# Kernel optimization log

Hardware: AMD Instinct MI355X
Metric: run time of the kernel (lower is better)

## Reference

```python
import jax, jax.numpy as jnp
import numpy as np

NUM_GROUPS = 32
NUM_HEADS = 8
EPS = 1e-5


def group_norm(x, gamma, beta):
    B, C, H, W = x.shape
    g = NUM_GROUPS
    xg = x.reshape(B, g, C // g, H, W)
    mean = xg.mean(axis=(2, 3, 4), keepdims=True)
    var = xg.var(axis=(2, 3, 4), keepdims=True)
    xn = ((xg - mean) * jax.lax.rsqrt(var + EPS)).reshape(B, C, H, W)
    return xn * gamma[None, :, None, None] + beta[None, :, None, None]


def setup_inputs() -> dict:
    key = jax.random.key(0)
    ks = jax.random.split(key, 7)
    B, C, H, W = 16, 512, 32, 32
    x = jax.random.normal(ks[0], (B, C, H, W), dtype=jnp.float32)
    norm_w = jnp.ones((C,), jnp.float32)
    norm_b = jnp.zeros((C,), jnp.float32)
    s1 = 1.0 / np.sqrt(C)
    qkv_w = jax.random.uniform(ks[1], (3 * C, C), jnp.float32, -s1, s1)
    qkv_b = jax.random.uniform(ks[2], (3 * C,), jnp.float32, -s1, s1)
    proj_w = jax.random.uniform(ks[3], (C, C), jnp.float32, -s1, s1)
    proj_b = jax.random.uniform(ks[4], (C,), jnp.float32, -s1, s1)
    return {"x": x, "norm_w": norm_w, "norm_b": norm_b,
            "qkv_w": qkv_w, "qkv_b": qkv_b,
            "proj_w": proj_w, "proj_b": proj_b}


def reference(x, norm_w, norm_b, qkv_w, qkv_b, proj_w, proj_b):
    B, C, H, W = x.shape
    nh = NUM_HEADS
    hd = C // nh
    S = H * W
    h = group_norm(x, norm_w, norm_b)
    # 1x1 conv == channel matmul: [B,3C,H,W]
    qkv = jnp.einsum('oc,bchw->bohw', qkv_w, h) + qkv_b[None, :, None, None]
    q, k, v = jnp.split(qkv, 3, axis=1)
    # q,v -> [B, nh, S, hd]; k -> [B, nh, hd, S]
    q = q.reshape(B, nh, hd, S).transpose(0, 1, 3, 2)
    k = k.reshape(B, nh, hd, S)
    v = v.reshape(B, nh, hd, S).transpose(0, 1, 3, 2)
    scale = 1.0 / np.sqrt(hd)
    attn = jnp.einsum('bhsd,bhdt->bhst', q, k) * scale
    attn = jax.nn.softmax(attn, axis=-1)
    out = jnp.einsum('bhst,bhtd->bhsd', attn, v)  # [B,nh,S,hd]
    out = out.transpose(0, 1, 3, 2).reshape(B, C, H, W)
    out = jnp.einsum('oc,bchw->bohw', proj_w, out) + proj_b[None, :, None, None]
    return out + x
```

## Files before the change

kernel.cpp:

```cpp
#include <hip/hip_runtime.h>
#include <hip/hip_bf16.h>
#include <stdint.h>

#define B_N 16
#define C_N 512
#define S_N 1024
#define G_N 32
#define NH  8
#define HD  64

typedef __attribute__((ext_vector_type(8))) short bf16x8;
typedef __attribute__((ext_vector_type(4))) float f32x4;
typedef __attribute__((ext_vector_type(16))) float f32x16;
typedef unsigned short u16;
typedef unsigned int   u32;
typedef __attribute__((ext_vector_type(4))) u16 u16x4;
typedef __attribute__((ext_vector_type(4))) u32 u32x4;

#define SC2F 0.18033688011112042f

__device__ __forceinline__ u16 f2bf(float f) {
  u32 u = __builtin_bit_cast(u32, f);
  u32 r = (u + 0x7fffu + ((u >> 16) & 1u)) >> 16;
  return (u16)r;
}

__device__ __forceinline__ u32 cvtpk(float a, float b) {
  u32 r;
  asm("v_cvt_pk_bf16_f32 %0, %1, %2" : "=v"(r) : "v"(a), "v"(b));
  return r;
}

__device__ __forceinline__ void gll16(const void* g, void* l) {
  __builtin_amdgcn_global_load_lds((const __attribute__((address_space(1))) u32*)g,
                                   (__attribute__((address_space(3))) u32*)l, 16, 0, 0);
}

__global__ __launch_bounds__(256) void gn_stats_cvt(const float* __restrict__ x,
                                                    float* __restrict__ stats,
                                                    const float* __restrict__ qkvw,
                                                    const float* __restrict__ projw,
                                                    u16* __restrict__ qw,
                                                    u16* __restrict__ pw) {
  const int blk = blockIdx.x;
  if (blk < 512) {
    const int bg = blk;
    const float4* xv = (const float4*)(x + (size_t)bg * (16 * S_N));
    float s = 0.f, ss = 0.f;
    for (int i = threadIdx.x; i < 4096; i += 256) {
      float4 v = xv[i];
      s  += v.x + v.y + v.z + v.w;
      ss += v.x*v.x + v.y*v.y + v.z*v.z + v.w*v.w;
    }
    #pragma unroll
    for (int m = 1; m < 64; m <<= 1) { s += __shfl_xor(s, m); ss += __shfl_xor(ss, m); }
    __shared__ float red[2][4];
    const int wid = threadIdx.x >> 6;
    if ((threadIdx.x & 63) == 0) { red[0][wid] = s; red[1][wid] = ss; }
    __syncthreads();
    if (threadIdx.x == 0) {
      float S1 = red[0][0]+red[0][1]+red[0][2]+red[0][3];
      float S2 = red[1][0]+red[1][1]+red[1][2]+red[1][3];
      float mean = S1 * (1.f/16384.f);
      float var  = S2 * (1.f/16384.f) - mean*mean;
      stats[bg*2]   = mean;
      stats[bg*2+1] = rsqrtf(var + 1e-5f);
    }
  } else {
    int i = (blk - 512)*256 + threadIdx.x;
    const float4* src; u16x4* dst; int j;
    if (i < 196608) { src = (const float4*)qkvw;  dst = (u16x4*)qw; j = i; }
    else            { src = (const float4*)projw; dst = (u16x4*)pw; j = i - 196608; }
    float4 v = src[j];
    u16x4 r = { f2bf(v.x), f2bf(v.y), f2bf(v.z), f2bf(v.w) };
    dst[j] = r;
  }
}

__global__ __launch_bounds__(256) void gn_apply_t(const float* __restrict__ x,
                                                  const float* __restrict__ stats,
                                                  const float* __restrict__ nw,
                                                  const float* __restrict__ nb,
                                                  u16* __restrict__ h_t) {
  const int c0 = blockIdx.x * 32, s0 = blockIdx.y * 64, b = blockIdx.z;
  __shared__ u16 tile[32][68];
  const int t = threadIdx.x;
  #pragma unroll
  for (int i = 0; i < 2; i++) {
    int idx4 = (i*256 + t) * 4;
    int cr = idx4 >> 6, sr = idx4 & 63;
    int c = c0 + cr;
    float4 v = *(const float4*)&x[((size_t)b*C_N + c)*S_N + s0 + sr];
    int bg = b*G_N + (c >> 4);
    float mean = stats[bg*2], rstd = stats[bg*2+1];
    float w = nw[c]*rstd;
    float bb = nb[c] - mean*w;
    tile[cr][sr]   = f2bf(v.x*w + bb);
    tile[cr][sr+1] = f2bf(v.y*w + bb);
    tile[cr][sr+2] = f2bf(v.z*w + bb);
    tile[cr][sr+3] = f2bf(v.w*w + bb);
  }
  __syncthreads();
  #pragma unroll
  for (int i = 0; i < 2; i++) {
    int idx = i*256 + t;
    int sr = idx >> 3;
    int cr4 = (idx & 7) * 4;
    u16x4 v = { tile[cr4][sr], tile[cr4+1][sr], tile[cr4+2][sr], tile[cr4+3][sr] };
    *(u16x4*)&h_t[((size_t)b*S_N + s0 + sr)*C_N + c0 + cr4] = v;
  }
}

__global__ __launch_bounds__(256) void gemm_qkv(const u16* __restrict__ h_t,
                                                const u16* __restrict__ wq,
                                                const float* __restrict__ bq,
                                                u16* __restrict__ Qp,
                                                u16* __restrict__ Kp,
                                                u16* __restrict__ Vp) {
  __shared__ u16 Ash[2][128*32];
  __shared__ u16 Bsh[2][128*32];
  const int n0 = blockIdx.x*128, m0 = blockIdx.y*128, b = blockIdx.z;
  const int tid = threadIdx.x, wid = tid >> 6, lane = tid & 63;
  const int wm = wid >> 1, wn = wid & 1;
  const u16* Ag = h_t + (size_t)b*S_N*C_N;
  const f32x4 vzero = {0.f,0.f,0.f,0.f};
  f32x4 acc[4][4];
  #pragma unroll
  for (int i=0;i<4;i++)
    #pragma unroll
    for (int j=0;j<4;j++) acc[i][j] = vzero;

  const int arow = lane >> 2, aslot = (lane & 3) * 8;

  auto stage = [&](u16* Adst, u16* Bdst, int k0s) {
    #pragma unroll
    for (int i = 0; i < 2; i++) {
      int r = wid*32 + i*16 + arow;
      gll16(Ag + (size_t)(m0+r)*C_N + k0s + aslot, &Adst[(wid*32+i*16)*32]);
      gll16(wq + (size_t)(n0+r)*C_N + k0s + aslot, &Bdst[(wid*32+i*16)*32]);
    }
  };
  auto compute = [&](const u16* AshC, const u16* BshC) {
    bf16x8 aF[4], bF[4];
    #pragma unroll
    for (int mi=0;mi<4;mi++)
      aF[mi] = *(const bf16x8*)&AshC[(wm*64+mi*16+(lane&15))*32 + (lane>>4)*8];
    #pragma unroll
    for (int ni=0;ni<4;ni++)
      bF[ni] = *(const bf16x8*)&BshC[(wn*64+ni*16+(lane&15))*32 + (lane>>4)*8];
    #pragma unroll
    for (int mi=0;mi<4;mi++)
      #pragma unroll
      for (int ni=0;ni<4;ni++)
        acc[mi][ni] = __builtin_amdgcn_mfma_f32_16x16x32_bf16(aF[mi], bF[ni], acc[mi][ni], 0, 0, 0);
  };

  stage(Ash[0], Bsh[0], 0);
  #pragma unroll 1
  for (int k0 = 0; k0 < C_N; k0 += 64) {
    asm volatile("s_waitcnt vmcnt(0)" ::: "memory");
    __syncthreads();
    stage(Ash[1], Bsh[1], k0 + 32);
    compute(Ash[0], Bsh[0]);
    asm volatile("s_waitcnt vmcnt(0)" ::: "memory");
    __syncthreads();
    if (k0 + 64 < C_N) stage(Ash[0], Bsh[0], k0 + 64);
    compute(Ash[1], Bsh[1]);
  }

  #pragma unroll
  for (int mi=0;mi<4;mi++) {
    #pragma unroll
    for (int ni=0;ni<4;ni++) {
      int o = n0 + wn*64 + ni*16 + (lane & 15);
      float bias = bq[o];
      int sec = o >> 9;
      int oo  = o & 511;
      int hh  = oo >> 6, d = oo & 63;
      size_t bh = (size_t)(b*NH + hh);
      float qsc = (sec == 0) ? SC2F : 1.0f;
      #pragma unroll
      for (int r=0;r<4;r++) {
        int s = m0 + wm*64 + mi*16 + (lane>>4)*4 + r;
        u16 bv = f2bf((acc[mi][ni][r] + bias) * qsc);
        if (sec == 0)      Qp[(bh*S_N + s)*HD + d] = bv;
        else if (sec == 1) Kp[(bh*S_N + s)*HD + d] = bv;
        else               Vp[(bh*HD + d)*S_N + s] = bv;
      }
    }
  }
}

__device__ __forceinline__ void attn_tile_body(const u16* __restrict__ Kb,
                                               const u16* __restrict__ Vb,
                                               const u16* __restrict__ KlC, const u16* __restrict__ VlC,
                                               u16* __restrict__ KlN, u16* __restrict__ VlN,
                                               const bf16x8 (&qf)[4], const bf16x8 onesf,
                                               f32x16 (&oacc)[2], f32x16& oacc_l,
                                               const int (&off)[2][4],
                                               int it, int hi,
                                               int ra, int rb, int ca, int cb, int wid) {
  const int t0 = it * 64;
  asm volatile("s_waitcnt vmcnt(0)" ::: "memory");
  __syncthreads();

  if (it < 15) {
    const int tn = t0 + 64;
    gll16(Kb + (size_t)(tn + ra)*HD + ca, &KlN[(wid*16    )*64]);
    gll16(Kb + (size_t)(tn + rb)*HD + cb, &KlN[(wid*16 + 8)*64]);
    gll16(Vb + (size_t)ra*S_N + tn + ca,  &VlN[(wid*16    )*64]);
    gll16(Vb + (size_t)rb*S_N + tn + cb,  &VlN[(wid*16 + 8)*64]);
  }

  bf16x8 kF[2][4];
  #pragma unroll
  for (int tt=0;tt<2;tt++)
    #pragma unroll
    for (int kt=0;kt<4;kt++)
      kF[tt][kt] = *(const bf16x8*)&KlC[off[tt][kt]];

  f32x16 st[2];
  #pragma unroll
  for (int tt=0;tt<2;tt++)
    #pragma unroll
    for (int i=0;i<16;i++) st[tt][i] = 0.f;
  __builtin_amdgcn_s_setprio(1);
  #pragma unroll
  for (int tt=0;tt<2;tt++)
    #pragma unroll
    for (int kt=0;kt<4;kt++)
      st[tt] = __builtin_amdgcn_mfma_f32_32x32x16_bf16(kF[tt][kt], qf[kt], st[tt], 0, 0, 0);
  __builtin_amdgcn_s_setprio(0);

  #pragma unroll
  for (int tt=0;tt<2;tt++)
    #pragma unroll
    for (int i=0;i<16;i++)
      st[tt][i] = exp2f(st[tt][i]);

  u32x4 paw[4];
  #pragma unroll
  for (int ks=0;ks<4;ks++) {
    u32 w0 = cvtpk(st[ks>>1][(ks&1)*8+0], st[ks>>1][(ks&1)*8+1]);
    u32 w1 = cvtpk(st[ks>>1][(ks&1)*8+2], st[ks>>1][(ks&1)*8+3]);
    u32 w2 = cvtpk(st[ks>>1][(ks&1)*8+4], st[ks>>1][(ks&1)*8+5]);
    u32 w3 = cvtpk(st[ks>>1][(ks&1)*8+6], st[ks>>1][(ks&1)*8+7]);
    asm("v_permlane32_swap_b32 %0, %1" : "+v"(w0), "+v"(w2));
    asm("v_permlane32_swap_b32 %0, %1" : "+v"(w1), "+v"(w3));
    u32x4 w = { w0, w1, w2, w3 };
    paw[ks] = w;
  }

  __builtin_amdgcn_s_setprio(1);
  #pragma unroll
  for (int ks=0;ks<4;ks++) {
    bf16x8 pb = __builtin_bit_cast(bf16x8, paw[ks]);
    oacc_l = __builtin_amdgcn_mfma_f32_32x32x16_bf16(onesf, pb, oacc_l, 0, 0, 0);
    #pragma unroll
    for (int dt=0;dt<2;dt++) {
      bf16x8 vF = *(const bf16x8*)&VlC[off[dt][ks]];
      oacc[dt] = __builtin_amdgcn_mfma_f32_32x32x16_bf16(vF, pb, oacc[dt], 0, 0, 0);
    }
  }
  __builtin_amdgcn_s_setprio(0);
}

__global__ __launch_bounds__(256) void attn_fwd(const u16* __restrict__ Qp,
                                                const u16* __restrict__ Kp,
                                                const u16* __restrict__ Vp,
                                                u16* __restrict__ at) {
  __shared__ u16 Kl[2][64*64];
  __shared__ u16 Vl[2][64*64];
  const int hh = blockIdx.x, q0 = blockIdx.y*128, b = blockIdx.z;
  const int tid = threadIdx.x, wid = tid >> 6, lane = tid & 63;
  const int l31 = lane & 31, hi = lane >> 5;
  const size_t bh = (size_t)(b*NH + hh);
  const u16* Qb = Qp + bh*(S_N*HD);
  const u16* Kb = Kp + bh*(S_N*HD);
  const u16* Vb = Vp + bh*(HD*S_N);
  const int s = q0 + wid*32 + l31;

  bf16x8 qf[4];
  #pragma unroll
  for (int kt=0;kt<4;kt++)
    qf[kt] = *(const bf16x8*)&Qb[(size_t)s*HD + kt*16 + hi*8];

  const u32x4 onesw = {0x3F803F80u, 0x3F803F80u, 0x3F803F80u, 0x3F803F80u};
  const bf16x8 onesf = __builtin_bit_cast(bf16x8, onesw);

  f32x16 oacc[2], oacc_l;
  #pragma unroll
  for (int dt=0;dt<2;dt++)
    #pragma unroll
    for (int i=0;i<16;i++) oacc[dt][i] = 0.f;
  #pragma unroll
  for (int i=0;i<16;i++) oacc_l[i] = 0.f;

  int off[2][4];
  #pragma unroll
  for (int g=0; g<2; g++)
    #pragma unroll
    for (int kt=0; kt<4; kt++) {
      int row = g*32 + l31;
      int phys = (kt*2 + hi) ^ (row & 7);
      off[g][kt] = row*64 + phys*8;
    }

  const int ra = wid*16 + (lane >> 3);
  const int rb = ra + 8;
  const int ca = (((lane & 7) ^ (ra & 7)) * 8);
  const int cb = (((lane & 7) ^ (rb & 7)) * 8);

  gll16(Kb + (size_t)ra*HD + ca,  &Kl[0][(wid*16    )*64]);
  gll16(Kb + (size_t)rb*HD + cb,  &Kl[0][(wid*16 + 8)*64]);
  gll16(Vb + (size_t)ra*S_N + ca, &Vl[0][(wid*16    )*64]);
  gll16(Vb + (size_t)rb*S_N + cb, &Vl[0][(wid*16 + 8)*64]);

  #pragma unroll 1
  for (int it = 0; it < 16; it += 2) {
    attn_tile_body(Kb, Vb, Kl[0], Vl[0], Kl[1], Vl[1], qf, onesf, oacc, oacc_l, off,
                   it,     hi, ra, rb, ca, cb, wid);
    attn_tile_body(Kb, Vb, Kl[1], Vl[1], Kl[0], Vl[0], qf, onesf, oacc, oacc_l, off,
                   it + 1, hi, ra, rb, ca, cb, wid);
  }

  float inv = 1.0f / oacc_l[0];
  #pragma unroll
  for (int dt=0;dt<2;dt++)
    #pragma unroll
    for (int qd=0;qd<4;qd++) {
      int dbase = 4*hi + 8*qd + 32*dt;
      u16x4 o;
      #pragma unroll
      for (int j=0;j<4;j++) o[j] = f2bf(oacc[dt][qd*4+j] * inv);
      *(u16x4*)&at[((size_t)b*S_N + s)*C_N + hh*HD + dbase] = o;
    }
}

__global__ __launch_bounds__(256) void gemm_proj(const u16* __restrict__ pwb,
                                                 const u16* __restrict__ at,
                                                 const float* __restrict__ bp,
                                                 const float* __restrict__ x,
                                                 float* __restrict__ out) {
  __shared__ u16 Ash[2][128*32];
  __shared__ u16 Bsh[2][128*32];
  const int n0 = blockIdx.x*128, m0 = blockIdx.y*128, b = blockIdx.z;
  const int tid = threadIdx.x, wid = tid >> 6, lane = tid & 63;
  const int wm = wid >> 1, wn = wid & 1;
  const u16* Bg = at + (size_t)b*S_N*C_N;
  const f32x4 vzero = {0.f,0.f,0.f,0.f};
  f32x4 acc[4][4];
  #pragma unroll
  for (int i=0;i<4;i++)
    #pragma unroll
    for (int j=0;j<4;j++) acc[i][j] = vzero;

  const int arow = lane >> 2, aslot = (lane & 3) * 8;

  auto stage = [&](u16* Adst, u16* Bdst, int k0s) {
    #pragma unroll
    for (int i = 0; i < 2; i++) {
      int r = wid*32 + i*16 + arow;
      gll16(pwb + (size_t)(m0+r)*C_N + k0s + aslot, &Adst[(wid*32+i*16)*32]);
      gll16(Bg  + (size_t)(n0+r)*C_N + k0s + aslot, &Bdst[(wid*32+i*16)*32]);
    }
  };
  auto compute = [&](const u16* AshC, const u16* BshC) {
    bf16x8 aF[4], bF[4];
    #pragma unroll
    for (int mi=0;mi<4;mi++)
      aF[mi] = *(const bf16x8*)&AshC[(wm*64+mi*16+(lane&15))*32 + (lane>>4)*8];
    #pragma unroll
    for (int ni=0;ni<4;ni++)
      bF[ni] = *(const bf16x8*)&BshC[(wn*64+ni*16+(lane&15))*32 + (lane>>4)*8];
    #pragma unroll
    for (int mi=0;mi<4;mi++)
      #pragma unroll
      for (int ni=0;ni<4;ni++)
        acc[mi][ni] = __builtin_amdgcn_mfma_f32_16x16x32_bf16(aF[mi], bF[ni], acc[mi][ni], 0, 0, 0);
  };

  stage(Ash[0], Bsh[0], 0);
  #pragma unroll 1
  for (int k0 = 0; k0 < C_N; k0 += 64) {
    asm volatile("s_waitcnt vmcnt(0)" ::: "memory");
    __syncthreads();
    stage(Ash[1], Bsh[1], k0 + 32);
    compute(Ash[0], Bsh[0]);
    asm volatile("s_waitcnt vmcnt(0)" ::: "memory");
    __syncthreads();
    if (k0 + 64 < C_N) stage(Ash[0], Bsh[0], k0 + 64);
    compute(Ash[1], Bsh[1]);
  }

  #pragma unroll
  for (int mi=0;mi<4;mi++) {
    #pragma unroll
    for (int ni=0;ni<4;ni++) {
      int ss = n0 + wn*64 + ni*16 + (lane & 15);
      #pragma unroll
      for (int r=0;r<4;r++) {
        int o = m0 + wm*64 + mi*16 + (lane>>4)*4 + r;
        size_t idx = ((size_t)b*C_N + o)*S_N + ss;
        out[idx] = acc[mi][ni][r] + bp[o] + x[idx];
      }
    }
  }
}

extern "C" void kernel_launch(void* const* d_in, const int* in_sizes, int n_in,
                              void* d_out, int out_size, void* d_ws, size_t ws_size,
                              hipStream_t stream) {
  const float* x     = (const float*)d_in[0];
  const float* nw    = (const float*)d_in[1];
  const float* nb    = (const float*)d_in[2];
  const float* qkvw  = (const float*)d_in[3];
  const float* qkvb  = (const float*)d_in[4];
  const float* projw = (const float*)d_in[5];
  const float* projb = (const float*)d_in[6];
  float* out = (float*)d_out;

  char* ws = (char*)d_ws;
  float* stats = (float*)ws;
  u16* h_t = (u16*)(ws + 4096);
  u16* qw  = (u16*)(ws + 4096 + 16777216);
  u16* pw  = (u16*)((char*)qw + 1572864);
  u16* Qp  = (u16*)((char*)pw + 524288);
  u16* Kp  = (u16*)((char*)Qp + 16777216);
  u16* Vp  = (u16*)((char*)Kp + 16777216);
  u16* at  = (u16*)((char*)Vp + 16777216);

  gn_stats_cvt<<<1536, 256, 0, stream>>>(x, stats, qkvw, projw, qw, pw);
  gn_apply_t  <<<dim3(16,16,16), 256, 0, stream>>>(x, stats, nw, nb, h_t);
  gemm_qkv    <<<dim3(12,8,16), 256, 0, stream>>>(h_t, qw, qkvb, Qp, Kp, Vp);
  attn_fwd    <<<dim3(8,8,16), 256, 0, stream>>>(Qp, Kp, Vp, at);
  gemm_proj   <<<dim3(8,4,16), 256, 0, stream>>>(pw, at, projb, x, out);
}
```

Baseline: 255.0 us.

## Triple-buffer GEMM LDS pipeline, XOR-swizzle LDS layout, and swizzle block order

```diff
diff --git a/kernel.cpp b/kernel.cpp
--- a/kernel.cpp
+++ b/kernel.cpp
@@ -117,9 +117,11 @@
                                                 u16* __restrict__ Qp,
                                                 u16* __restrict__ Kp,
                                                 u16* __restrict__ Vp) {
-  __shared__ u16 Ash[2][128*32];
-  __shared__ u16 Bsh[2][128*32];
-  const int n0 = blockIdx.x*128, m0 = blockIdx.y*128, b = blockIdx.z;
+  __shared__ u16 Ash[3][128*32];
+  __shared__ u16 Bsh[3][128*32];
+  const int lin = blockIdx.x + blockIdx.y*12 + blockIdx.z*96;
+  const int swz = (lin & 7)*192 + (lin >> 3);
+  const int n0 = (swz % 12)*128, m0 = ((swz/12) & 7)*128, b = swz/96;
   const int tid = threadIdx.x, wid = tid >> 6, lane = tid & 63;
   const int wm = wid >> 1, wn = wid & 1;
   const u16* Ag = h_t + (size_t)b*S_N*C_N;
@@ -130,24 +132,31 @@
     #pragma unroll
     for (int j=0;j<4;j++) acc[i][j] = vzero;
 
-  const int arow = lane >> 2, aslot = (lane & 3) * 8;
+  const int arow = lane >> 2;
+  const int cs = (((lane & 3) ^ ((lane >> 2) & 3)) * 8);
+  int offA[4], offB[4];
+  #pragma unroll
+  for (int f=0; f<4; f++) {
+    int rowa = wm*64 + f*16 + (lane & 15);
+    int rowb = wn*64 + f*16 + (lane & 15);
+    offA[f] = rowa*32 + (((lane>>4) ^ (rowa & 3))*8);
+    offB[f] = rowb*32 + (((lane>>4) ^ (rowb & 3))*8);
+  }
 
   auto stage = [&](u16* Adst, u16* Bdst, int k0s) {
     #pragma unroll
     for (int i = 0; i < 2; i++) {
       int r = wid*32 + i*16 + arow;
-      gll16(Ag + (size_t)(m0+r)*C_N + k0s + aslot, &Adst[(wid*32+i*16)*32]);
-      gll16(wq + (size_t)(n0+r)*C_N + k0s + aslot, &Bdst[(wid*32+i*16)*32]);
+      gll16(Ag + (size_t)(m0+r)*C_N + k0s + cs, Adst + (wid*32+i*16)*32);
+      gll16(wq + (size_t)(n0+r)*C_N + k0s + cs, Bdst + (wid*32+i*16)*32);
     }
   };
   auto compute = [&](const u16* AshC, const u16* BshC) {
     bf16x8 aF[4], bF[4];
     #pragma unroll
-    for (int mi=0;mi<4;mi++)
-      aF[mi] = *(const bf16x8*)&AshC[(wm*64+mi*16+(lane&15))*32 + (lane>>4)*8];
-    #pragma unroll
-    for (int ni=0;ni<4;ni++)
-      bF[ni] = *(const bf16x8*)&BshC[(wn*64+ni*16+(lane&15))*32 + (lane>>4)*8];
+    for (int mi=0;mi<4;mi++) aF[mi] = *(const bf16x8*)&AshC[offA[mi]];
+    #pragma unroll
+    for (int ni=0;ni<4;ni++) bF[ni] = *(const bf16x8*)&BshC[offB[ni]];
     #pragma unroll
     for (int mi=0;mi<4;mi++)
       #pragma unroll
@@ -155,18 +164,23 @@
         acc[mi][ni] = __builtin_amdgcn_mfma_f32_16x16x32_bf16(aF[mi], bF[ni], acc[mi][ni], 0, 0, 0);
   };
 
-  stage(Ash[0], Bsh[0], 0);
+  u16 *A0=&Ash[0][0], *A1=&Ash[1][0], *A2=&Ash[2][0];
+  u16 *B0=&Bsh[0][0], *B1=&Bsh[1][0], *B2=&Bsh[2][0];
+  stage(A0, B0, 0);
+  stage(A1, B1, 32);
   #pragma unroll 1
-  for (int k0 = 0; k0 < C_N; k0 += 64) {
-    asm volatile("s_waitcnt vmcnt(0)" ::: "memory");
+  for (int i = 0; i < 15; i++) {
+    asm volatile("s_waitcnt vmcnt(4)" ::: "memory");
     __syncthreads();
-    stage(Ash[1], Bsh[1], k0 + 32);
-    compute(Ash[0], Bsh[0]);
-    asm volatile("s_waitcnt vmcnt(0)" ::: "memory");
-    __syncthreads();
-    if (k0 + 64 < C_N) stage(Ash[0], Bsh[0], k0 + 64);
-    compute(Ash[1], Bsh[1]);
-  }
+    if (i < 14) stage(A2, B2, (i+2)*32);
+    compute(A0, B0);
+    u16* t;
+    t=A0; A0=A1; A1=A2; A2=t;
+    t=B0; B0=B1; B1=B2; B2=t;
+  }
+  asm volatile("s_waitcnt vmcnt(0)" ::: "memory");
+  __syncthreads();
+  compute(A0, B0);
 
   #pragma unroll
   for (int mi=0;mi<4;mi++) {
@@ -342,9 +356,11 @@
                                                  const float* __restrict__ bp,
                                                  const float* __restrict__ x,
                                                  float* __restrict__ out) {
-  __shared__ u16 Ash[2][128*32];
-  __shared__ u16 Bsh[2][128*32];
-  const int n0 = blockIdx.x*128, m0 = blockIdx.y*128, b = blockIdx.z;
+  __shared__ u16 Ash[3][128*32];
+  __shared__ u16 Bsh[3][128*32];
+  const int lin = blockIdx.x + blockIdx.y*8 + blockIdx.z*32;
+  const int swz = (lin & 7)*64 + (lin >> 3);
+  const int n0 = (swz & 7)*128, m0 = ((swz >> 3) & 3)*128, b = swz >> 5;
   const int tid = threadIdx.x, wid = tid >> 6, lane = tid & 63;
   const int wm = wid >> 1, wn = wid & 1;
   const u16* Bg = at + (size_t)b*S_N*C_N;
@@ -355,24 +371,31 @@
     #pragma unroll
     for (int j=0;j<4;j++) acc[i][j] = vzero;
 
-  const int arow = lane >> 2, aslot = (lane & 3) * 8;
+  const int arow = lane >> 2;
+  const int cs = (((lane & 3) ^ ((lane >> 2) & 3)) * 8);
+  int offA[4], offB[4];
+  #pragma unroll
+  for (int f=0; f<4; f++) {
+    int rowa = wm*64 + f*16 + (lane & 15);
+    int rowb = wn*64 + f*16 + (lane & 15);
+    offA[f] = rowa*32 + (((lane>>4) ^ (rowa & 3))*8);
+    offB[f] = rowb*32 + (((lane>>4) ^ (rowb & 3))*8);
+  }
 
   auto stage = [&](u16* Adst, u16* Bdst, int k0s) {
     #pragma unroll
     for (int i = 0; i < 2; i++) {
       int r = wid*32 + i*16 + arow;
-      gll16(pwb + (size_t)(m0+r)*C_N + k0s + aslot, &Adst[(wid*32+i*16)*32]);
-      gll16(Bg  + (size_t)(n0+r)*C_N + k0s + aslot, &Bdst[(wid*32+i*16)*32]);
+      gll16(pwb + (size_t)(m0+r)*C_N + k0s + cs, Adst + (wid*32+i*16)*32);
+      gll16(Bg  + (size_t)(n0+r)*C_N + k0s + cs, Bdst + (wid*32+i*16)*32);
     }
   };
   auto compute = [&](const u16* AshC, const u16* BshC) {
     bf16x8 aF[4], bF[4];
     #pragma unroll
-    for (int mi=0;mi<4;mi++)
-      aF[mi] = *(const bf16x8*)&AshC[(wm*64+mi*16+(lane&15))*32 + (lane>>4)*8];
-    #pragma unroll
-    for (int ni=0;ni<4;ni++)
-      bF[ni] = *(const bf16x8*)&BshC[(wn*64+ni*16+(lane&15))*32 + (lane>>4)*8];
+    for (int mi=0;mi<4;mi++) aF[mi] = *(const bf16x8*)&AshC[offA[mi]];
+    #pragma unroll
+    for (int ni=0;ni<4;ni++) bF[ni] = *(const bf16x8*)&BshC[offB[ni]];
     #pragma unroll
     for (int mi=0;mi<4;mi++)
       #pragma unroll
@@ -380,18 +403,23 @@
         acc[mi][ni] = __builtin_amdgcn_mfma_f32_16x16x32_bf16(aF[mi], bF[ni], acc[mi][ni], 0, 0, 0);
   };
 
-  stage(Ash[0], Bsh[0], 0);
+  u16 *A0=&Ash[0][0], *A1=&Ash[1][0], *A2=&Ash[2][0];
+  u16 *B0=&Bsh[0][0], *B1=&Bsh[1][0], *B2=&Bsh[2][0];
+  stage(A0, B0, 0);
+  stage(A1, B1, 32);
   #pragma unroll 1
-  for (int k0 = 0; k0 < C_N; k0 += 64) {
-    asm volatile("s_waitcnt vmcnt(0)" ::: "memory");
+  for (int i = 0; i < 15; i++) {
+    asm volatile("s_waitcnt vmcnt(4)" ::: "memory");
     __syncthreads();
-    stage(Ash[1], Bsh[1], k0 + 32);
-    compute(Ash[0], Bsh[0]);
-    asm volatile("s_waitcnt vmcnt(0)" ::: "memory");
-    __syncthreads();
-    if (k0 + 64 < C_N) stage(Ash[0], Bsh[0], k0 + 64);
-    compute(Ash[1], Bsh[1]);
-  }
+    if (i < 14) stage(A2, B2, (i+2)*32);
+    compute(A0, B0);
+    u16* t;
+    t=A0; A0=A1; A1=A2; A2=t;
+    t=B0; B0=B1; B1=B2; B2=t;
+  }
+  asm volatile("s_waitcnt vmcnt(0)" ::: "memory");
+  __syncthreads();
+  compute(A0, B0);
 
   #pragma unroll
   for (int mi=0;mi<4;mi++) {
```

After: 248.4 us. 1.03x faster.
